# Kernel optimization log

Measured on AMD Instinct MI355X. Metric: run time of the kernel, lower is better.

Reference implementation:

```python
import jax, jax.numpy as jnp
import numpy as np

N, E, D_IN, L, H, U = 20000, 320000, 256, 4, 4, 64
HID = H * U  # 256
OUT = 64
LN_EPS = 1e-3  # keras LayerNormalization default epsilon
NEG_SLOPE = 0.2


def layer_norm(x, g, b):
    m = jnp.mean(x, axis=-1, keepdims=True)
    v = jnp.var(x, axis=-1, keepdims=True)
    return (x - m) * jax.lax.rsqrt(v + LN_EPS) * g + b


def gatv2(x, dst, src, Wl, Wr, a):
    # x: [N, HID]; Wl/Wr: [HID, H, U]; a: [H, U]
    zl = jnp.einsum('nd,dhu->nhu', x, Wl)  # target projection
    zr = jnp.einsum('nd,dhu->nhu', x, Wr)  # source projection / messages
    f = jax.nn.leaky_relu(zl[dst] + zr[src], NEG_SLOPE)       # [E, H, U]
    s = jnp.einsum('ehu,hu->eh', f, a)                        # [E, H]
    smax = jax.ops.segment_max(s, dst, num_segments=N)        # [N, H]
    es = jnp.exp(s - smax[dst])
    denom = jax.ops.segment_sum(es, dst, num_segments=N)      # [N, H]
    agg = jax.ops.segment_sum(es[:, :, None] * zr[src], dst, num_segments=N)
    agg = agg / (denom[:, :, None] + 1e-9)                    # [N, H, U]
    return agg.reshape(N, HID) + x  # residual (input dim == H*U)


def setup_inputs() -> dict:
    key = jax.random.key(0)
    ks = jax.random.split(key, 10)
    s_in = 1.0 / np.sqrt(D_IN)
    s_h = 1.0 / np.sqrt(HID)
    return {
        'x': jax.random.normal(ks[0], (N, D_IN), jnp.float32),
        'head_W': jax.random.normal(ks[1], (D_IN, HID), jnp.float32) * s_in,
        'head_b': jnp.zeros((HID,), jnp.float32),
        'ng_g': jnp.ones((L, HID), jnp.float32),
        'ng_b': jnp.zeros((L, HID), jnp.float32),
        'Wl': jax.random.normal(ks[2], (L, HID, H, U), jnp.float32) * s_h,
        'Wr': jax.random.normal(ks[3], (L, HID, H, U), jnp.float32) * s_h,
        'att': jax.random.normal(ks[4], (L, H, U), jnp.float32) * (1.0 / np.sqrt(U)),
        'nd_g': jnp.ones((L, HID), jnp.float32),
        'nd_b': jnp.zeros((L, HID), jnp.float32),
        'dense_W': jax.random.normal(ks[5], (L, HID, 4 * HID), jnp.float32) * s_h,
        'dense_b': jnp.zeros((L, 4 * HID), jnp.float32),
        'tail_W': jax.random.normal(ks[6], (HID, OUT), jnp.float32) * s_h,
        'tail_b': jnp.zeros((OUT,), jnp.float32),
        'edges': jax.random.randint(ks[7], (E, 2), 0, N, jnp.int32),
    }


def reference(x, head_W, head_b, ng_g, ng_b, Wl, Wr, att, nd_g, nd_b,
              dense_W, dense_b, tail_W, tail_b, edges):
    dst, src = edges[:, 0], edges[:, 1]
    h = x @ head_W + head_b  # head_layer
    for l in range(L):
        h = layer_norm(h, ng_g[l], ng_b[l])
        h = gatv2(h, dst, src, Wl[l], Wr[l], att[l])
        xr = layer_norm(h, nd_g[l], nd_b[l])
        # inference: dropout is identity
        d = jax.nn.gelu(xr @ dense_W[l] + dense_b[l], approximate=True)  # [N, 4*HID]
        h = d.reshape(N, 4, HID).sum(axis=1) + xr  # Add(split(.,4)) + residual
    return h @ tail_W + tail_b
```

## Files before the change

kernel.cpp:

```cpp
#include <hip/hip_runtime.h>
#include <cstdint>

#define NN 20000
#define EE 320000
#define DHID 256

typedef short bf16x8 __attribute__((ext_vector_type(8)));
typedef float f32x4 __attribute__((ext_vector_type(4)));


__device__ __forceinline__ float b2f(unsigned short u) {
    union { unsigned int i; float f; } v;
    v.i = ((unsigned int)u) << 16;
    return v.f;
}

__device__ __forceinline__ void b2f2(unsigned int w, float& lo, float& hi) {
    union { unsigned int i; float f; } a, c;
    a.i = w << 16;
    c.i = w & 0xffff0000u;
    lo = a.f;
    hi = c.f;
}

__device__ __forceinline__ unsigned short f2b(float x) {
    union { float f; unsigned int i; } v;
    v.f = x;
    unsigned int r = (v.i + 0x7FFFu + ((v.i >> 16) & 1u)) >> 16;
    return (unsigned short)r;
}

__device__ __forceinline__ float wave_sum(float v) {
#pragma unroll
    for (int m = 1; m < 64; m <<= 1) v += __shfl_xor(v, m);
    return v;
}

__device__ __forceinline__ float quad16_sum(float v) {
#pragma unroll
    for (int m = 1; m < 16; m <<= 1) v += __shfl_xor(v, m);
    return v;
}

__device__ __forceinline__ float gelu_f(float x) {
    float z = 0.7978845608028654f * (x + 0.044715f * x * x * x);
    float e = __expf(2.0f * z);
    float t = 1.0f - 2.0f / (e + 1.0f);
    return 0.5f * x * (1.0f + t);
}

__device__ __forceinline__ void gld16(const unsigned short* g, unsigned short* lds) {
    __builtin_amdgcn_global_load_lds((const __attribute__((address_space(1))) unsigned int*)g,
                                     (__attribute__((address_space(3))) unsigned int*)lds, 16, 0, 0);
}


__global__ void hist_kernel(const int* __restrict__ edges, int* __restrict__ counts, int E_) {
    int e = blockIdx.x * 256 + threadIdx.x;
    if (e >= E_) return;
    atomicAdd(&counts[edges[e * 2]], 1);
}

__global__ __launch_bounds__(1024) void scan_block(const int* __restrict__ counts,
                                                   int* __restrict__ excl,
                                                   int* __restrict__ bsums, int n) {
    __shared__ int sd[1024];
    int tid = threadIdx.x;
    int i = blockIdx.x * 1024 + tid;
    int c = (i < n) ? counts[i] : 0;
    sd[tid] = c;
    __syncthreads();
#pragma unroll
    for (int off = 1; off < 1024; off <<= 1) {
        int v = (tid >= off) ? sd[tid - off] : 0;
        __syncthreads();
        sd[tid] += v;
        __syncthreads();
    }
    if (i < n) excl[i] = sd[tid] - c;
    if (tid == 1023) bsums[blockIdx.x] = sd[1023];
}

__global__ void scan_tops(int* __restrict__ bsums, int nb) {
    if (threadIdx.x == 0 && blockIdx.x == 0) {
        int run = 0;
        for (int i = 0; i < nb; ++i) { int t = bsums[i]; bsums[i] = run; run += t; }
    }
}

__global__ void scan_fix(const int* __restrict__ excl, const int* __restrict__ bsums,
                         int* __restrict__ indptr, int* __restrict__ cursor, int n) {
    int i = blockIdx.x * 256 + threadIdx.x;
    if (i < n) {
        int v = excl[i] + bsums[i >> 10];
        indptr[i] = v;
        cursor[i] = v;
    }
    if (i == 0) indptr[n] = EE;
}

__global__ void scatter_kernel(const int* __restrict__ edges, int* __restrict__ cursor,
                               int* __restrict__ ssrc, int E_) {
    int e = blockIdx.x * 256 + threadIdx.x;
    if (e >= E_) return;
    int dstn = edges[e * 2];
    int src  = edges[e * 2 + 1];
    int pos = atomicAdd(&cursor[dstn], 1);
    ssrc[pos] = src;
}


__global__ __launch_bounds__(256) void transpose_bf16(const float* __restrict__ W,
                                                      unsigned short* __restrict__ Wt,
                                                      int K, int M, size_t lsW, size_t lsT) {
    W  += (size_t)blockIdx.z * lsW;
    Wt += (size_t)blockIdx.z * lsT;
    __shared__ float sm[32][33];
    int m0 = blockIdx.x * 32, k0 = blockIdx.y * 32;
    int tx = threadIdx.x & 31, ty = threadIdx.x >> 5;
#pragma unroll
    for (int i = 0; i < 4; ++i)
        sm[ty + i * 8][tx] = W[(size_t)(k0 + ty + i * 8) * M + m0 + tx];
    __syncthreads();
#pragma unroll
    for (int i = 0; i < 4; ++i)
        Wt[(size_t)(m0 + ty + i * 8) * K + k0 + tx] = f2b(sm[tx][ty + i * 8]);
}

__global__ __launch_bounds__(256) void transpose_perm(const float* __restrict__ W,
                                                      unsigned short* __restrict__ Wt,
                                                      int K, int M, size_t lsW, size_t lsT) {
    W  += (size_t)blockIdx.z * lsW;
    Wt += (size_t)blockIdx.z * lsT;
    __shared__ float sm[32][33];
    int m0 = blockIdx.x * 32, k0 = blockIdx.y * 32;
    int tx = threadIdx.x & 31, ty = threadIdx.x >> 5;
#pragma unroll
    for (int i = 0; i < 4; ++i)
        sm[ty + i * 8][tx] = W[(size_t)(k0 + ty + i * 8) * M + m0 + tx];
    __syncthreads();
#pragma unroll
    for (int i = 0; i < 4; ++i) {
        int mm = m0 + ty + i * 8;
        int c = mm >> 8, j = mm & 255;
        int by = j >> 5, t = j & 31;
        int cc = (by << 7) | ((t >> 4) << 6) | (c << 4) | (t & 15);
        Wt[(size_t)cc * K + k0 + tx] = f2b(sm[tx][ty + i * 8]);
    }
}

__global__ void convert_bf16(const float* __restrict__ in, unsigned short* __restrict__ out, int n4) {
    int i = blockIdx.x * 256 + threadIdx.x;
    if (i >= n4) return;
    float4 v = *(const float4*)(in + (size_t)i * 4);
    ushort4 o;
    o.x = f2b(v.x); o.y = f2b(v.y); o.z = f2b(v.z); o.w = f2b(v.w);
    *(ushort4*)(out + (size_t)i * 4) = o;
}


__global__ __launch_bounds__(256) void ln_kernel(const float* __restrict__ X,
                                                 const float* __restrict__ g,
                                                 const float* __restrict__ b,
                                                 unsigned short* __restrict__ Yb, int nrows) {
    int row = blockIdx.x * 4 + (threadIdx.x >> 6);
    int lane = threadIdx.x & 63;
    if (row >= nrows) return;
    float4 v = *(const float4*)(X + (size_t)row * DHID + lane * 4);
    float sum = wave_sum(v.x + v.y + v.z + v.w);
    float sq  = wave_sum(v.x * v.x + v.y * v.y + v.z * v.z + v.w * v.w);
    float mean = sum * (1.0f / DHID);
    float var  = sq * (1.0f / DHID) - mean * mean;
    float r = rsqrtf(fmaxf(var, 0.0f) + 1e-3f);
    float4 gv = *(const float4*)(g + lane * 4);
    float4 bv = *(const float4*)(b + lane * 4);
    float4 o;
    o.x = (v.x - mean) * r * gv.x + bv.x;
    o.y = (v.y - mean) * r * gv.y + bv.y;
    o.z = (v.z - mean) * r * gv.z + bv.z;
    o.w = (v.w - mean) * r * gv.w + bv.w;
    ushort4 ob;
    ob.x = f2b(o.x); ob.y = f2b(o.y); ob.z = f2b(o.z); ob.w = f2b(o.w);
    *(ushort4*)(Yb + (size_t)row * DHID + lane * 4) = ob;
}

__global__ __launch_bounds__(256) void ln_dense(const unsigned short* __restrict__ d,
                                                const unsigned short* __restrict__ xrb,
                                                const float* __restrict__ g,
                                                const float* __restrict__ b,
                                                unsigned short* __restrict__ Yb, int nrows) {
    int row = blockIdx.x * 4 + (threadIdx.x >> 6);
    int lane = threadIdx.x & 63;
    if (row >= nrows) return;
    ushort4 xu = *(const ushort4*)(xrb + (size_t)row * DHID + lane * 4);
    ushort4 du = *(const ushort4*)(d   + (size_t)row * DHID + lane * 4);
    float4 v;
    v.x = b2f(xu.x) + b2f(du.x);
    v.y = b2f(xu.y) + b2f(du.y);
    v.z = b2f(xu.z) + b2f(du.z);
    v.w = b2f(xu.w) + b2f(du.w);
    float sum = wave_sum(v.x + v.y + v.z + v.w);
    float sq  = wave_sum(v.x * v.x + v.y * v.y + v.z * v.z + v.w * v.w);
    float mean = sum * (1.0f / DHID);
    float var  = sq * (1.0f / DHID) - mean * mean;
    float r = rsqrtf(fmaxf(var, 0.0f) + 1e-3f);
    float4 gv = *(const float4*)(g + lane * 4);
    float4 bv = *(const float4*)(b + lane * 4);
    float4 o;
    o.x = (v.x - mean) * r * gv.x + bv.x;
    o.y = (v.y - mean) * r * gv.y + bv.y;
    o.z = (v.z - mean) * r * gv.z + bv.z;
    o.w = (v.w - mean) * r * gv.w + bv.w;
    ushort4 ob;
    ob.x = f2b(o.x); ob.y = f2b(o.y); ob.z = f2b(o.z); ob.w = f2b(o.w);
    *(ushort4*)(Yb + (size_t)row * DHID + lane * 4) = ob;
}

__global__ __launch_bounds__(256) void combine_final(const unsigned short* __restrict__ d,
                                                     const unsigned short* __restrict__ xrb,
                                                     unsigned short* __restrict__ hb, int nrows) {
    int row = blockIdx.x * 4 + (threadIdx.x >> 6);
    int lane = threadIdx.x & 63;
    if (row >= nrows) return;
    ushort4 xu = *(const ushort4*)(xrb + (size_t)row * DHID + lane * 4);
    ushort4 du = *(const ushort4*)(d   + (size_t)row * DHID + lane * 4);
    ushort4 ob;
    ob.x = f2b(b2f(xu.x) + b2f(du.x));
    ob.y = f2b(b2f(xu.y) + b2f(du.y));
    ob.z = f2b(b2f(xu.z) + b2f(du.z));
    ob.w = f2b(b2f(xu.w) + b2f(du.w));
    *(ushort4*)(hb + (size_t)row * DHID + lane * 4) = ob;
}


#define CS_STRIDE 140
#define CS2_STRIDE 40

template <int EP>
__global__ __launch_bounds__(256, 3) void gemm128(const unsigned short* __restrict__ A,
                                                  const unsigned short* __restrict__ B,
                                                  const float* __restrict__ bias,
                                                  void* __restrict__ Cv, int nrows, int ncols) {
    __shared__ unsigned short smem[128 * CS_STRIDE];
    unsigned short* As = smem;
    unsigned short* Bs = smem + 8192;
    unsigned short* Cs = smem;
    const int bm = blockIdx.x * 128, bn = blockIdx.y * 128;
    if (bm >= nrows) return;
    const int tid  = threadIdx.x;
    const int w    = tid >> 6, lane = tid & 63;
    const int quad = lane >> 4, l16 = lane & 15;
    const int wm = w >> 1, wn = w & 1;

    const int srow = lane & 15;
    const int sg   = lane >> 4;
    int ga0 = min(bm + w * 32 + srow,      nrows - 1);
    int ga1 = min(bm + w * 32 + 16 + srow, nrows - 1);
    int gb0 = min(bn + w * 32 + srow,      ncols - 1);
    int gb1 = min(bn + w * 32 + 16 + srow, ncols - 1);
    const unsigned short* Ap0 = A + (size_t)ga0 * 256 + sg * 8;
    const unsigned short* Ap1 = A + (size_t)ga1 * 256 + sg * 8;
    const unsigned short* Bp0 = B + (size_t)gb0 * 256 + sg * 8;
    const unsigned short* Bp1 = B + (size_t)gb1 * 256 + sg * 8;
    unsigned short* la0 = As + (2 * w) * 1024;
    unsigned short* la1 = As + (2 * w + 1) * 1024;
    unsigned short* lb0 = Bs + (2 * w) * 1024;
    unsigned short* lb1 = Bs + (2 * w + 1) * 1024;

    f32x4 acc[4][4] = {};
    for (int k0 = 0; k0 < 256; k0 += 64) {
        gld16(Ap0 + k0,      la0);
        gld16(Ap0 + k0 + 32, la0 + 512);
        gld16(Ap1 + k0,      la1);
        gld16(Ap1 + k0 + 32, la1 + 512);
        gld16(Bp0 + k0,      lb0);
        gld16(Bp0 + k0 + 32, lb0 + 512);
        gld16(Bp1 + k0,      lb1);
        gld16(Bp1 + k0 + 32, lb1 + 512);
        __syncthreads();
#pragma unroll
        for (int kk = 0; kk < 2; ++kk) {
            bf16x8 a[4], b[4];
#pragma unroll
            for (int mi = 0; mi < 4; ++mi)
                a[mi] = *(const bf16x8*)(As + (wm * 4 + mi) * 1024 + (kk * 4 + quad) * 128 + l16 * 8);
#pragma unroll
            for (int ni = 0; ni < 4; ++ni)
                b[ni] = *(const bf16x8*)(Bs + (wn * 4 + ni) * 1024 + (kk * 4 + quad) * 128 + l16 * 8);
#pragma unroll
            for (int mi = 0; mi < 4; ++mi)
#pragma unroll
                for (int ni = 0; ni < 4; ++ni)
                    acc[mi][ni] = __builtin_amdgcn_mfma_f32_16x16x32_bf16(a[mi], b[ni], acc[mi][ni], 0, 0, 0);
        }
        __syncthreads();
    }

    if (EP == 0) {
#pragma unroll
        for (int ni = 0; ni < 4; ++ni) {
            int col = bn + wn * 64 + ni * 16 + l16;
            if (col >= ncols) continue;
            float bv = bias ? bias[col] : 0.0f;
#pragma unroll
            for (int mi = 0; mi < 4; ++mi) {
#pragma unroll
                for (int r = 0; r < 4; ++r) {
                    int row = bm + wm * 64 + mi * 16 + quad * 4 + r;
                    if (row < nrows) ((float*)Cv)[(size_t)row * ncols + col] = acc[mi][ni][r] + bv;
                }
            }
        }
    } else if (EP == 1) {
#pragma unroll
        for (int ni = 0; ni < 4; ++ni) {
            int lc = wn * 64 + ni * 16 + l16;
#pragma unroll
            for (int mi = 0; mi < 4; ++mi) {
#pragma unroll
                for (int r = 0; r < 4; ++r) {
                    int lr = wm * 64 + mi * 16 + quad * 4 + r;
                    Cs[lr * CS_STRIDE + lc] = f2b(acc[mi][ni][r]);
                }
            }
        }
        __syncthreads();
#pragma unroll
        for (int i = 0; i < 8; ++i) {
            int id = tid + 256 * i;
            int lr = id >> 4;
            int lc = (id & 15) * 8;
            int grow = bm + lr;
            if (grow < nrows) {
                uint4 val = *(const uint4*)(Cs + lr * CS_STRIDE + lc);
                *(uint4*)((unsigned short*)Cv + (size_t)grow * ncols + bn + lc) = val;
            }
        }
    } else {
        unsigned short* Cs2 = smem;
        int jfl = wn * 16 + l16;
        int jf  = (bn >> 2) + jfl;
        float bv0 = bias[jf];
        float bv1 = bias[256 + jf];
        float bv2 = bias[512 + jf];
        float bv3 = bias[768 + jf];
#pragma unroll
        for (int mi = 0; mi < 4; ++mi) {
#pragma unroll
            for (int r = 0; r < 4; ++r) {
                float v = gelu_f(acc[mi][0][r] + bv0) + gelu_f(acc[mi][1][r] + bv1)
                        + gelu_f(acc[mi][2][r] + bv2) + gelu_f(acc[mi][3][r] + bv3);
                int lr = wm * 64 + mi * 16 + quad * 4 + r;
                Cs2[lr * CS2_STRIDE + jfl] = f2b(v);
            }
        }
        __syncthreads();
#pragma unroll
        for (int i = 0; i < 2; ++i) {
            int id = tid + 256 * i;
            int lr = id >> 2;
            int q  = id & 3;
            int grow = bm + lr;
            if (grow < nrows) {
                uint4 val = *(const uint4*)(Cs2 + lr * CS2_STRIDE + q * 8);
                *(uint4*)((unsigned short*)Cv + (size_t)grow * 256 + (bn >> 2) + q * 8) = val;
            }
        }
    }
}


__global__ __launch_bounds__(256) void gat_fused(const unsigned short* __restrict__ zb,
                                                 const float* __restrict__ att,
                                                 const int* __restrict__ ssrc,
                                                 const int* __restrict__ indptr,
                                                 const unsigned short* __restrict__ hnb,
                                                 const float* __restrict__ g,
                                                 const float* __restrict__ b,
                                                 unsigned short* __restrict__ xrb, int nrows) {
    int wid = threadIdx.x >> 6;
    int lane = threadIdx.x & 63;
    int n = blockIdx.x * 4 + wid;
    if (n >= nrows) return;
    int start = indptr[n];
    int end = indptr[n + 1];

    ushort4 zlu = *(const ushort4*)(zb + (size_t)n * 512 + lane * 4);
    float zl0 = b2f(zlu.x), zl1 = b2f(zlu.y), zl2 = b2f(zlu.z), zl3 = b2f(zlu.w);
    float4 a4 = *(const float4*)(att + lane * 4);
    size_t idx = (size_t)n * DHID + lane * 4;
    ushort4 ru = *(const ushort4*)(hnb + idx);
    float rr0 = b2f(ru.x), rr1 = b2f(ru.y), rr2 = b2f(ru.z), rr3 = b2f(ru.w);

    float denom = 0.f;
    float ax = 0.f, ay = 0.f, az = 0.f, aw = 0.f;

    const uint2* zrp = (const uint2*)(zb + 256);
    uint2 c0 = make_uint2(0, 0), c1 = make_uint2(0, 0);
    uint2 c2 = make_uint2(0, 0), c3 = make_uint2(0, 0);
    uint2 c4 = make_uint2(0, 0), c5 = make_uint2(0, 0);
    uint2 c6 = make_uint2(0, 0), c7 = make_uint2(0, 0);
    if (start < end) {
        int e1 = end - 1;
        c0 = zrp[(size_t)ssrc[start] * 128 + lane];
        c1 = zrp[(size_t)ssrc[min(start + 1, e1)] * 128 + lane];
        c2 = zrp[(size_t)ssrc[min(start + 2, e1)] * 128 + lane];
        c3 = zrp[(size_t)ssrc[min(start + 3, e1)] * 128 + lane];
        c4 = zrp[(size_t)ssrc[min(start + 4, e1)] * 128 + lane];
        c5 = zrp[(size_t)ssrc[min(start + 5, e1)] * 128 + lane];
        c6 = zrp[(size_t)ssrc[min(start + 6, e1)] * 128 + lane];
        c7 = zrp[(size_t)ssrc[min(start + 7, e1)] * 128 + lane];
    }
    for (int p = start; p < end; p += 4) {
        uint2 u0 = c0, u1 = c1, u2 = c2, u3 = c3;
        c0 = c4; c1 = c5; c2 = c6; c3 = c7;
        if (p + 8 < end) {
            int e1 = end - 1;
            c4 = zrp[(size_t)ssrc[p + 8] * 128 + lane];
            c5 = zrp[(size_t)ssrc[min(p + 9,  e1)] * 128 + lane];
            c6 = zrp[(size_t)ssrc[min(p + 10, e1)] * 128 + lane];
            c7 = zrp[(size_t)ssrc[min(p + 11, e1)] * 128 + lane];
        }
        float z00, z01, z02, z03, z10, z11, z12, z13;
        float z20, z21, z22, z23, z30, z31, z32, z33;
        b2f2(u0.x, z00, z01); b2f2(u0.y, z02, z03);
        b2f2(u1.x, z10, z11); b2f2(u1.y, z12, z13);
        b2f2(u2.x, z20, z21); b2f2(u2.y, z22, z23);
        b2f2(u3.x, z30, z31); b2f2(u3.y, z32, z33);

        float v00 = zl0 + z00, v01 = zl1 + z01, v02 = zl2 + z02, v03 = zl3 + z03;
        float v10 = zl0 + z10, v11 = zl1 + z11, v12 = zl2 + z12, v13 = zl3 + z13;
        float v20 = zl0 + z20, v21 = zl1 + z21, v22 = zl2 + z22, v23 = zl3 + z23;
        float v30 = zl0 + z30, v31 = zl1 + z31, v32 = zl2 + z32, v33 = zl3 + z33;
        v00 = fmaxf(v00, 0.2f * v00); v01 = fmaxf(v01, 0.2f * v01);
        v02 = fmaxf(v02, 0.2f * v02); v03 = fmaxf(v03, 0.2f * v03);
        v10 = fmaxf(v10, 0.2f * v10); v11 = fmaxf(v11, 0.2f * v11);
        v12 = fmaxf(v12, 0.2f * v12); v13 = fmaxf(v13, 0.2f * v13);
        v20 = fmaxf(v20, 0.2f * v20); v21 = fmaxf(v21, 0.2f * v21);
        v22 = fmaxf(v22, 0.2f * v22); v23 = fmaxf(v23, 0.2f * v23);
        v30 = fmaxf(v30, 0.2f * v30); v31 = fmaxf(v31, 0.2f * v31);
        v32 = fmaxf(v32, 0.2f * v32); v33 = fmaxf(v33, 0.2f * v33);
        float p0 = a4.x * v00 + a4.y * v01 + a4.z * v02 + a4.w * v03;
        float p1 = a4.x * v10 + a4.y * v11 + a4.z * v12 + a4.w * v13;
        float p2 = a4.x * v20 + a4.y * v21 + a4.z * v22 + a4.w * v23;
        float p3 = a4.x * v30 + a4.y * v31 + a4.z * v32 + a4.w * v33;
        float s0 = quad16_sum(p0);
        float s1 = quad16_sum(p1);
        float s2 = quad16_sum(p2);
        float s3 = quad16_sum(p3);
        bool b1 = (p + 1 < end), b2 = (p + 2 < end), b3 = (p + 3 < end);
        float w0 = __expf(s0);
        float w1 = b1 ? __expf(s1) : 0.0f;
        float w2 = b2 ? __expf(s2) : 0.0f;
        float w3 = b3 ? __expf(s3) : 0.0f;
        denom += (w0 + w1) + (w2 + w3);
        ax += (w0 * z00 + w1 * z10) + (w2 * z20 + w3 * z30);
        ay += (w0 * z01 + w1 * z11) + (w2 * z21 + w3 * z31);
        az += (w0 * z02 + w1 * z12) + (w2 * z22 + w3 * z32);
        aw += (w0 * z03 + w1 * z13) + (w2 * z23 + w3 * z33);
    }
    float inv = 1.0f / (denom + 1e-9f);
    float4 o;
    o.x = ax * inv + rr0;
    o.y = ay * inv + rr1;
    o.z = az * inv + rr2;
    o.w = aw * inv + rr3;
    float sum = wave_sum(o.x + o.y + o.z + o.w);
    float sq  = wave_sum(o.x * o.x + o.y * o.y + o.z * o.z + o.w * o.w);
    float mean = sum * (1.0f / DHID);
    float var  = sq * (1.0f / DHID) - mean * mean;
    float rnorm = rsqrtf(fmaxf(var, 0.0f) + 1e-3f);
    float4 gv = *(const float4*)(g + lane * 4);
    float4 bv = *(const float4*)(b + lane * 4);
    float4 y;
    y.x = (o.x - mean) * rnorm * gv.x + bv.x;
    y.y = (o.y - mean) * rnorm * gv.y + bv.y;
    y.z = (o.z - mean) * rnorm * gv.z + bv.z;
    y.w = (o.w - mean) * rnorm * gv.w + bv.w;
    ushort4 ob;
    ob.x = f2b(y.x); ob.y = f2b(y.y); ob.z = f2b(y.z); ob.w = f2b(y.w);
    *(ushort4*)(xrb + idx) = ob;
}


extern "C" void kernel_launch(void* const* d_in, const int* in_sizes, int n_in,
                              void* d_out, int out_size, void* d_ws, size_t ws_size,
                              hipStream_t stream) {
    const float* x       = (const float*)d_in[0];
    const float* head_W  = (const float*)d_in[1];
    const float* head_b  = (const float*)d_in[2];
    const float* ng_g    = (const float*)d_in[3];
    const float* ng_b    = (const float*)d_in[4];
    const float* Wl      = (const float*)d_in[5];
    const float* Wr      = (const float*)d_in[6];
    const float* att     = (const float*)d_in[7];
    const float* nd_g    = (const float*)d_in[8];
    const float* nd_b    = (const float*)d_in[9];
    const float* dense_W = (const float*)d_in[10];
    const float* dense_b = (const float*)d_in[11];
    const float* tail_W  = (const float*)d_in[12];
    const float* tail_b  = (const float*)d_in[13];
    const int*   edges   = (const int*)d_in[14];
    float* out = (float*)d_out;

    const size_t NH = (size_t)NN * DHID;
    float* xr = (float*)d_ws;
    float* hn = xr + NH;
    unsigned short* hnb = (unsigned short*)(hn + NH);
    unsigned short* xrb = hnb + NH;
    unsigned short* U   = xrb + NH;
    unsigned short* zb  = U;
    unsigned short* d_buf = U;
    unsigned short* headT  = U + 4 * NH;
    unsigned short* WzT    = headT + 65536;
    unsigned short* denseT = WzT + 524288;
    unsigned short* tailT  = denseT + 1048576;
    int* counts = (int*)(tailT + 16384);
    int* bsums  = counts + NN;
    int* excl   = bsums + 32;
    int* indptr = excl + NN;
    int* cursor = indptr + NN + 1;
    int* ssrc   = cursor + NN;

    hipMemsetAsync(counts, 0, NN * sizeof(int), stream);
    hist_kernel<<<(EE + 255) / 256, 256, 0, stream>>>(edges, counts, EE);
    scan_block<<<(NN + 1023) / 1024, 1024, 0, stream>>>(counts, excl, bsums, NN);
    scan_tops<<<1, 64, 0, stream>>>(bsums, (NN + 1023) / 1024);
    scan_fix<<<(NN + 255) / 256, 256, 0, stream>>>(excl, bsums, indptr, cursor, NN);
    scatter_kernel<<<(EE + 255) / 256, 256, 0, stream>>>(edges, cursor, ssrc, EE);

    transpose_bf16<<<dim3(8, 8, 1), 256, 0, stream>>>(head_W, headT, 256, 256, 0, 0);
    transpose_bf16<<<dim3(8, 8, 4), 256, 0, stream>>>(Wl, WzT, 256, 256, 65536, 131072);
    transpose_bf16<<<dim3(8, 8, 4), 256, 0, stream>>>(Wr, WzT + 65536, 256, 256, 65536, 131072);
    transpose_perm<<<dim3(32, 8, 4), 256, 0, stream>>>(dense_W, denseT, 256, 1024, 262144, 262144);
    transpose_bf16<<<dim3(2, 8, 1), 256, 0, stream>>>(tail_W, tailT, 256, 64, 0, 0);
    convert_bf16<<<(int)(NH / 4 + 255) / 256, 256, 0, stream>>>(x, hnb, (int)(NH / 4));

    const int GXP = 160;
    gemm128<0><<<dim3(GXP, 2), 256, 0, stream>>>(hnb, headT, head_b, xr, NN, 256);

    for (int l = 0; l < 4; ++l) {
        if (l == 0)
            ln_kernel<<<NN / 4, 256, 0, stream>>>(xr, ng_g, ng_b, hnb, NN);
        else
            ln_dense<<<NN / 4, 256, 0, stream>>>(d_buf, xrb, ng_g + l * 256, ng_b + l * 256, hnb, NN);
        gemm128<1><<<dim3(GXP, 4), 256, 0, stream>>>(hnb, WzT + (size_t)l * 131072, nullptr, zb, NN, 512);
        gat_fused<<<(NN + 3) / 4, 256, 0, stream>>>(zb, att + l * 256, ssrc, indptr, hnb,
                                                    nd_g + l * 256, nd_b + l * 256, xrb, NN);
        gemm128<3><<<dim3(GXP, 8), 256, 0, stream>>>(xrb, denseT + (size_t)l * 262144,
                                                     dense_b + l * 1024, d_buf, NN, 1024);
    }
    combine_final<<<NN / 4, 256, 0, stream>>>(d_buf, xrb, hnb, NN);
    gemm128<0><<<dim3(GXP, 1), 256, 0, stream>>>(hnb, tailT, tail_b, out, NN, 64);
}
```

Before: 552.7 us.

## Pad CSR segments to multiples of four and store pre-scaled byte offsets

Each node's edge segment in the CSR is padded to a multiple of four entries, and the stored value is the source index pre-shifted into a byte offset. The GAT kernel can then fetch four offsets with one aligned 16-byte load, with no min() clamping and no 64-bit index multiply. The gather loop is restructured into two alternating register buffers of four edges each, and the residual load moves after the loop. Padding entries are zeroed so they point at row 0 and are masked out, at the cost of a larger memset and an extra pad_counts kernel.

```diff
diff --git a/kernel.cpp b/kernel.cpp
--- a/kernel.cpp
+++ b/kernel.cpp
@@ -59,6 +59,11 @@
     int e = blockIdx.x * 256 + threadIdx.x;
     if (e >= E_) return;
     atomicAdd(&counts[edges[e * 2]], 1);
+}
+
+__global__ void pad_counts(const int* __restrict__ counts, int* __restrict__ pc, int n) {
+    int i = blockIdx.x * 256 + threadIdx.x;
+    if (i < n) pc[i] = (counts[i] + 3) & ~3;
 }
 
 __global__ __launch_bounds__(1024) void scan_block(const int* __restrict__ counts,
@@ -88,25 +93,27 @@
     }
 }
 
-__global__ void scan_fix(const int* __restrict__ excl, const int* __restrict__ bsums,
-                         int* __restrict__ indptr, int* __restrict__ cursor, int n) {
+__global__ void scan_fix2(const int* __restrict__ excl, const int* __restrict__ bsums,
+                          const int* __restrict__ counts,
+                          int* __restrict__ astart, int* __restrict__ aend,
+                          int* __restrict__ cursor, int n) {
     int i = blockIdx.x * 256 + threadIdx.x;
     if (i < n) {
         int v = excl[i] + bsums[i >> 10];
-        indptr[i] = v;
+        astart[i] = v;
         cursor[i] = v;
-    }
-    if (i == 0) indptr[n] = EE;
-}
-
-__global__ void scatter_kernel(const int* __restrict__ edges, int* __restrict__ cursor,
-                               int* __restrict__ ssrc, int E_) {
+        aend[i]   = v + counts[i];
+    }
+}
+
+__global__ void scatter2(const int* __restrict__ edges, int* __restrict__ cursor,
+                         unsigned int* __restrict__ soff, int E_) {
     int e = blockIdx.x * 256 + threadIdx.x;
     if (e >= E_) return;
     int dstn = edges[e * 2];
     int src  = edges[e * 2 + 1];
     int pos = atomicAdd(&cursor[dstn], 1);
-    ssrc[pos] = src;
+    soff[pos] = (unsigned int)src << 10;
 }
 
 
@@ -372,8 +379,9 @@
 
 __global__ __launch_bounds__(256) void gat_fused(const unsigned short* __restrict__ zb,
                                                  const float* __restrict__ att,
-                                                 const int* __restrict__ ssrc,
-                                                 const int* __restrict__ indptr,
+                                                 const unsigned int* __restrict__ soff,
+                                                 const int* __restrict__ astart,
+                                                 const int* __restrict__ aend,
                                                  const unsigned short* __restrict__ hnb,
                                                  const float* __restrict__ g,
                                                  const float* __restrict__ b,
@@ -382,45 +390,20 @@
     int lane = threadIdx.x & 63;
     int n = blockIdx.x * 4 + wid;
     if (n >= nrows) return;
-    int start = indptr[n];
-    int end = indptr[n + 1];
+    int p0  = astart[n];
+    int end = aend[n];
 
     ushort4 zlu = *(const ushort4*)(zb + (size_t)n * 512 + lane * 4);
     float zl0 = b2f(zlu.x), zl1 = b2f(zlu.y), zl2 = b2f(zlu.z), zl3 = b2f(zlu.w);
     float4 a4 = *(const float4*)(att + lane * 4);
-    size_t idx = (size_t)n * DHID + lane * 4;
-    ushort4 ru = *(const ushort4*)(hnb + idx);
-    float rr0 = b2f(ru.x), rr1 = b2f(ru.y), rr2 = b2f(ru.z), rr3 = b2f(ru.w);
+
+    const char* zrb = (const char*)zb + 512;
+    const unsigned int loff = (unsigned int)lane * 8u;
 
     float denom = 0.f;
     float ax = 0.f, ay = 0.f, az = 0.f, aw = 0.f;
 
-    const uint2* zrp = (const uint2*)(zb + 256);
-    uint2 c0 = make_uint2(0, 0), c1 = make_uint2(0, 0);
-    uint2 c2 = make_uint2(0, 0), c3 = make_uint2(0, 0);
-    uint2 c4 = make_uint2(0, 0), c5 = make_uint2(0, 0);
-    uint2 c6 = make_uint2(0, 0), c7 = make_uint2(0, 0);
-    if (start < end) {
-        int e1 = end - 1;
-        c0 = zrp[(size_t)ssrc[start] * 128 + lane];
-        c1 = zrp[(size_t)ssrc[min(start + 1, e1)] * 128 + lane];
-        c2 = zrp[(size_t)ssrc[min(start + 2, e1)] * 128 + lane];
-        c3 = zrp[(size_t)ssrc[min(start + 3, e1)] * 128 + lane];
-        c4 = zrp[(size_t)ssrc[min(start + 4, e1)] * 128 + lane];
-        c5 = zrp[(size_t)ssrc[min(start + 5, e1)] * 128 + lane];
-        c6 = zrp[(size_t)ssrc[min(start + 6, e1)] * 128 + lane];
-        c7 = zrp[(size_t)ssrc[min(start + 7, e1)] * 128 + lane];
-    }
-    for (int p = start; p < end; p += 4) {
-        uint2 u0 = c0, u1 = c1, u2 = c2, u3 = c3;
-        c0 = c4; c1 = c5; c2 = c6; c3 = c7;
-        if (p + 8 < end) {
-            int e1 = end - 1;
-            c4 = zrp[(size_t)ssrc[p + 8] * 128 + lane];
-            c5 = zrp[(size_t)ssrc[min(p + 9,  e1)] * 128 + lane];
-            c6 = zrp[(size_t)ssrc[min(p + 10, e1)] * 128 + lane];
-            c7 = zrp[(size_t)ssrc[min(p + 11, e1)] * 128 + lane];
-        }
+    auto edge4 = [&](uint2 u0, uint2 u1, uint2 u2, uint2 u3, int pb) {
         float z00, z01, z02, z03, z10, z11, z12, z13;
         float z20, z21, z22, z23, z30, z31, z32, z33;
         b2f2(u0.x, z00, z01); b2f2(u0.y, z02, z03);
@@ -440,31 +423,60 @@
         v22 = fmaxf(v22, 0.2f * v22); v23 = fmaxf(v23, 0.2f * v23);
         v30 = fmaxf(v30, 0.2f * v30); v31 = fmaxf(v31, 0.2f * v31);
         v32 = fmaxf(v32, 0.2f * v32); v33 = fmaxf(v33, 0.2f * v33);
-        float p0 = a4.x * v00 + a4.y * v01 + a4.z * v02 + a4.w * v03;
-        float p1 = a4.x * v10 + a4.y * v11 + a4.z * v12 + a4.w * v13;
-        float p2 = a4.x * v20 + a4.y * v21 + a4.z * v22 + a4.w * v23;
-        float p3 = a4.x * v30 + a4.y * v31 + a4.z * v32 + a4.w * v33;
-        float s0 = quad16_sum(p0);
-        float s1 = quad16_sum(p1);
-        float s2 = quad16_sum(p2);
-        float s3 = quad16_sum(p3);
-        bool b1 = (p + 1 < end), b2 = (p + 2 < end), b3 = (p + 3 < end);
+        float q0 = a4.x * v00 + a4.y * v01 + a4.z * v02 + a4.w * v03;
+        float q1 = a4.x * v10 + a4.y * v11 + a4.z * v12 + a4.w * v13;
+        float q2 = a4.x * v20 + a4.y * v21 + a4.z * v22 + a4.w * v23;
+        float q3 = a4.x * v30 + a4.y * v31 + a4.z * v32 + a4.w * v33;
+        float s0 = quad16_sum(q0);
+        float s1 = quad16_sum(q1);
+        float s2 = quad16_sum(q2);
+        float s3 = quad16_sum(q3);
         float w0 = __expf(s0);
-        float w1 = b1 ? __expf(s1) : 0.0f;
-        float w2 = b2 ? __expf(s2) : 0.0f;
-        float w3 = b3 ? __expf(s3) : 0.0f;
+        float w1 = (pb + 1 < end) ? __expf(s1) : 0.0f;
+        float w2 = (pb + 2 < end) ? __expf(s2) : 0.0f;
+        float w3 = (pb + 3 < end) ? __expf(s3) : 0.0f;
         denom += (w0 + w1) + (w2 + w3);
         ax += (w0 * z00 + w1 * z10) + (w2 * z20 + w3 * z30);
         ay += (w0 * z01 + w1 * z11) + (w2 * z21 + w3 * z31);
         az += (w0 * z02 + w1 * z12) + (w2 * z22 + w3 * z32);
         aw += (w0 * z03 + w1 * z13) + (w2 * z23 + w3 * z33);
-    }
+    };
+
+    uint4 oA = *(const uint4*)(soff + p0);
+    uint2 cA0 = *(const uint2*)(zrb + (oA.x + loff));
+    uint2 cA1 = *(const uint2*)(zrb + (oA.y + loff));
+    uint2 cA2 = *(const uint2*)(zrb + (oA.z + loff));
+    uint2 cA3 = *(const uint2*)(zrb + (oA.w + loff));
+    uint4 oB = *(const uint4*)(soff + p0 + 4);
+    uint2 cB0 = *(const uint2*)(zrb + (oB.x + loff));
+    uint2 cB1 = *(const uint2*)(zrb + (oB.y + loff));
+    uint2 cB2 = *(const uint2*)(zrb + (oB.z + loff));
+    uint2 cB3 = *(const uint2*)(zrb + (oB.w + loff));
+
+    for (int p = p0; p < end; p += 8) {
+        edge4(cA0, cA1, cA2, cA3, p);
+        oA = *(const uint4*)(soff + p + 8);
+        cA0 = *(const uint2*)(zrb + (oA.x + loff));
+        cA1 = *(const uint2*)(zrb + (oA.y + loff));
+        cA2 = *(const uint2*)(zrb + (oA.z + loff));
+        cA3 = *(const uint2*)(zrb + (oA.w + loff));
+        if (p + 4 >= end) break;
+        edge4(cB0, cB1, cB2, cB3, p + 4);
+        oB = *(const uint4*)(soff + p + 12);
+        cB0 = *(const uint2*)(zrb + (oB.x + loff));
+        cB1 = *(const uint2*)(zrb + (oB.y + loff));
+        cB2 = *(const uint2*)(zrb + (oB.z + loff));
+        cB3 = *(const uint2*)(zrb + (oB.w + loff));
+    }
+
+    size_t idx = (size_t)n * DHID + lane * 4;
+    ushort4 ru = *(const ushort4*)(hnb + idx);
     float inv = 1.0f / (denom + 1e-9f);
     float4 o;
-    o.x = ax * inv + rr0;
-    o.y = ay * inv + rr1;
-    o.z = az * inv + rr2;
-    o.w = aw * inv + rr3;
+    o.x = ax * inv + b2f(ru.x);
+    o.y = ay * inv + b2f(ru.y);
+    o.z = az * inv + b2f(ru.z);
+    o.w = aw * inv + b2f(ru.w);
     float sum = wave_sum(o.x + o.y + o.z + o.w);
     float sq  = wave_sum(o.x * o.x + o.y * o.y + o.z * o.z + o.w * o.w);
     float mean = sum * (1.0f / DHID);
@@ -504,6 +516,7 @@
     float* out = (float*)d_out;
 
     const size_t NH = (size_t)NN * DHID;
+    const int SOFF_LEN = EE + 4 * NN + 16;
     float* xr = (float*)d_ws;
     float* hn = xr + NH;
     unsigned short* hnb = (unsigned short*)(hn + NH);
@@ -515,19 +528,23 @@
     unsigned short* WzT    = headT + 65536;
     unsigned short* denseT = WzT + 524288;
     unsigned short* tailT  = denseT + 1048576;
-    int* counts = (int*)(tailT + 16384);
-    int* bsums  = counts + NN;
-    int* excl   = bsums + 32;
-    int* indptr = excl + NN;
-    int* cursor = indptr + NN + 1;
-    int* ssrc   = cursor + NN;
+    int* counts  = (int*)(tailT + 16384);
+    int* pcounts = counts + NN;
+    int* bsums   = pcounts + NN;
+    int* excl    = bsums + 32;
+    int* cursor  = excl + NN;
+    unsigned int* soff = (unsigned int*)hn;
+    int* astart = (int*)(soff + SOFF_LEN);
+    int* aendp  = astart + NN;
 
     hipMemsetAsync(counts, 0, NN * sizeof(int), stream);
+    hipMemsetAsync(soff, 0, SOFF_LEN * sizeof(int), stream);
     hist_kernel<<<(EE + 255) / 256, 256, 0, stream>>>(edges, counts, EE);
-    scan_block<<<(NN + 1023) / 1024, 1024, 0, stream>>>(counts, excl, bsums, NN);
+    pad_counts<<<(NN + 255) / 256, 256, 0, stream>>>(counts, pcounts, NN);
+    scan_block<<<(NN + 1023) / 1024, 1024, 0, stream>>>(pcounts, excl, bsums, NN);
     scan_tops<<<1, 64, 0, stream>>>(bsums, (NN + 1023) / 1024);
-    scan_fix<<<(NN + 255) / 256, 256, 0, stream>>>(excl, bsums, indptr, cursor, NN);
-    scatter_kernel<<<(EE + 255) / 256, 256, 0, stream>>>(edges, cursor, ssrc, EE);
+    scan_fix2<<<(NN + 255) / 256, 256, 0, stream>>>(excl, bsums, counts, astart, aendp, cursor, NN);
+    scatter2<<<(EE + 255) / 256, 256, 0, stream>>>(edges, cursor, soff, EE);
 
     transpose_bf16<<<dim3(8, 8, 1), 256, 0, stream>>>(head_W, headT, 256, 256, 0, 0);
     transpose_bf16<<<dim3(8, 8, 4), 256, 0, stream>>>(Wl, WzT, 256, 256, 65536, 131072);
@@ -545,7 +562,7 @@
         else
             ln_dense<<<NN / 4, 256, 0, stream>>>(d_buf, xrb, ng_g + l * 256, ng_b + l * 256, hnb, NN);
         gemm128<1><<<dim3(GXP, 4), 256, 0, stream>>>(hnb, WzT + (size_t)l * 131072, nullptr, zb, NN, 512);
-        gat_fused<<<(NN + 3) / 4, 256, 0, stream>>>(zb, att + l * 256, ssrc, indptr, hnb,
+        gat_fused<<<(NN + 3) / 4, 256, 0, stream>>>(zb, att + l * 256, soff, astart, aendp, hnb,
                                                     nd_g + l * 256, nd_b + l * 256, xrb, NN);
         gemm128<3><<<dim3(GXP, 8), 256, 0, stream>>>(xrb, denseT + (size_t)l * 262144,
                                                      dense_b + l * 1024, d_buf, NN, 1024);
```

Result: no change. 544.7 us (-1.5%).
